# Optimization experiments

Hardware: AMD Instinct MI355X
Metric: run time of the kernel (lower is better)

## Reference

```python
import jax, jax.numpy as jnp
import numpy as np

NDIGIT = 10
DIM_IN = 256
DIM_OUT = 784
BATCH = 16384


def setup_inputs() -> dict:
    key = jax.random.key(0)
    k_theta, k_label, k_W = jax.random.split(key, 3)
    theta = jax.random.normal(k_theta, (BATCH, DIM_IN), dtype=jnp.float32)
    label = jax.random.randint(k_label, (BATCH,), 0, NDIGIT, dtype=jnp.int32)
    # xavier_uniform for each (dim_out, dim_in) matrix
    limit = float(np.sqrt(6.0 / (DIM_IN + DIM_OUT)))
    megaW = jax.random.uniform(k_W, (NDIGIT, DIM_OUT, DIM_IN), dtype=jnp.float32,
                               minval=-limit, maxval=limit)
    megab = jnp.zeros((NDIGIT, DIM_OUT), dtype=jnp.float32)
    return {"theta": theta, "label": label, "megaW": megaW, "megab": megab}


def reference(theta, label, megaW, megab):
    # Dense compute across all 10 digit experts (matches torch.bmm over repeated theta)
    # added: [b, ndigit, dim_out]
    added = jnp.einsum('ndi,bi->bnd', megaW, theta) + megab[None, :, :]
    # Select the expert output per example by label (vector_gather)
    selected = jnp.take_along_axis(added, label[:, None, None].astype(jnp.int32), axis=1)[:, 0, :]
    probs = jax.nn.sigmoid(selected)
    return probs
```

## Files before the change

kernel.cpp:

```cpp
#include <hip/hip_runtime.h>
#include <hip/hip_bf16.h>

#define NDIGIT 10
#define DIM_IN 256
#define DIM_OUT 784
#define BATCH 16384
#define BM 64
#define BN 112
#define NCB 7
#define MAX_MT (BATCH / BM + NDIGIT)
#define G_BLOCKS (MAX_MT * NCB)
#define QB 14336
#define RBSTRIDE 116
#define LDS_BYTES 29696

#define WS_IDX 1024
#define WS_DESC 600
#define WS_WBF_BYTES 69632
#define WS_TH_BYTES (WS_WBF_BYTES + 2007040 * 2)
#define WS_NEED (WS_TH_BYTES + BATCH * DIM_IN * 2)

typedef __attribute__((ext_vector_type(4))) float f32x4;
typedef __attribute__((ext_vector_type(8))) short bf16x8;

__device__ __forceinline__ short f2bf(float f) {
    union { float f; unsigned u; } c; c.f = f;
    unsigned u = c.u;
    u += 0x7fffu + ((u >> 16) & 1u);
    return (short)(u >> 16);
}

__device__ __forceinline__ void gload16(const void* gp, void* lp) {
    __builtin_amdgcn_global_load_lds(
        (const __attribute__((address_space(1))) void*)gp,
        (__attribute__((address_space(3))) void*)lp, 16, 0, 0);
}

__global__ void hist_k(const int* __restrict__ label, int* __restrict__ wsi) {
    __shared__ int h[NDIGIT];
    int j = blockIdx.x, t = threadIdx.x;
    if (t < NDIGIT) h[t] = 0;
    __syncthreads();
    int i0 = j * 512;
    atomicAdd(&h[label[i0 + t]], 1);
    atomicAdd(&h[label[i0 + 256 + t]], 1);
    __syncthreads();
    if (t < NDIGIT) wsi[64 + j * 16 + t] = h[t];
}

__global__ void scatter2_k(const int* __restrict__ label, int* __restrict__ wsi) {
    __shared__ int tot[NDIGIT], bef[NDIGIT], base[NDIGIT + 1], cur[NDIGIT], toff[NDIGIT + 1];
    int j = blockIdx.x, t = threadIdx.x;
    if (t < NDIGIT) {
        int s = 0, sb = 0;
        for (int jj = 0; jj < 32; ++jj) {
            int v = wsi[64 + jj * 16 + t];
            s += v;
            if (jj < j) sb += v;
        }
        tot[t] = s; bef[t] = sb;
    }
    __syncthreads();
    if (t == 0) {
        int off = 0, tf = 0;
        for (int g = 0; g < NDIGIT; ++g) {
            base[g] = off; toff[g] = tf;
            off += tot[g]; tf += (tot[g] + BM - 1) / BM;
        }
        base[NDIGIT] = off; toff[NDIGIT] = tf;
    }
    __syncthreads();
    if (t < NDIGIT) cur[t] = base[t] + bef[t];
    if (j == 0) {
        int ptotal = toff[NDIGIT];
        for (int p = t; p < ptotal; p += 512) {
            int g2 = 0;
            while (p >= toff[g2 + 1]) ++g2;
            int row0 = (p - toff[g2]) * BM;
            int rcv = tot[g2] - row0; if (rcv > BM) rcv = BM;
            wsi[WS_DESC + p] = (base[g2] + row0) | (rcv << 14) | (g2 << 21);
        }
        if (t < NDIGIT) { wsi[t] = base[t]; wsi[12 + t] = toff[t]; }
        if (t == 0) {
            wsi[10] = base[NDIGIT]; wsi[22] = toff[NDIGIT]; wsi[24] = toff[NDIGIT];
        }
    }
    __syncthreads();
    int i = j * 512 + t;
    int g = label[i];
    int r = atomicAdd(&cur[g], 1);
    wsi[WS_IDX + r] = i;
}

__global__ void gw_k(const float* __restrict__ theta,
                     const float* __restrict__ megaW,
                     const int* __restrict__ wsi,
                     short* __restrict__ thsort,
                     short* __restrict__ wbf) {
    int b = blockIdx.x, t = threadIdx.x;
    if (b < 2048) {
        int gid = b * 256 + t;
        int r = gid >> 5;
        int c8 = (gid & 31) << 3;
        int src = wsi[WS_IDX + r];
        const float* p = theta + (size_t)src * DIM_IN + c8;
        f32x4 v0 = *(const f32x4*)p;
        f32x4 v1 = *(const f32x4*)(p + 4);
        bf16x8 o;
        o[0] = f2bf(v0[0]); o[1] = f2bf(v0[1]); o[2] = f2bf(v0[2]); o[3] = f2bf(v0[3]);
        o[4] = f2bf(v1[0]); o[5] = f2bf(v1[1]); o[6] = f2bf(v1[2]); o[7] = f2bf(v1[3]);
        *(bf16x8*)(thsort + (size_t)r * DIM_IN + c8) = o;
    } else {
        int base = (b - 2048) * 2048 + t * 8;
        f32x4 v0 = *(const f32x4*)(megaW + base);
        f32x4 v1 = *(const f32x4*)(megaW + base + 4);
        bf16x8 o;
        o[0] = f2bf(v0[0]); o[1] = f2bf(v0[1]); o[2] = f2bf(v0[2]); o[3] = f2bf(v0[3]);
        o[4] = f2bf(v1[0]); o[5] = f2bf(v1[1]); o[6] = f2bf(v1[2]); o[7] = f2bf(v1[3]);
        *(bf16x8*)(wbf + base) = o;
    }
}

__device__ __forceinline__ void stage_q(const char* Wcb, int q, char* Bq, int tid) {
#pragma unroll
    for (int it = 0; it < 4; ++it) {
        int chunk = it * 256 + tid;
        if (chunk >= 896) chunk -= 128;
        int lbyte = chunk << 4;
        int L = lbyte ^ ((((lbyte >> 7) & 7)) << 4);
        int row = L >> 7, koff = L & 127;
        gload16(Wcb + row * 512 + q * 128 + koff, Bq + lbyte);
    }
}

#define COMPUTE_Q(Q, BUF) do {                                                 \
    _Pragma("unroll")                                                          \
    for (int ksl = 0; ksl < 2; ++ksl) {                                        \
        _Pragma("unroll")                                                      \
        for (int ns = 0; ns < NCB; ++ns) {                                     \
            int n_ = ns * 16 + r16;                                            \
            int byte_ = (n_ << 7) + (ksl << 6) + (kg << 4);                    \
            byte_ ^= (n_ & 7) << 4;                                            \
            bf16x8 bfr_ = *(const bf16x8*)((const char*)(BUF) + byte_);        \
            acc[ns] = __builtin_amdgcn_mfma_f32_16x16x32_bf16(                 \
                a[(Q) * 2 + ksl], bfr_, acc[ns], 0, 0, 0);                     \
        }                                                                      \
    }                                                                          \
} while (0)

__launch_bounds__(256, 4)
__global__ void moe_gemm11_k(const short* __restrict__ thsort,
                             const float* __restrict__ megab,
                             const int* __restrict__ wsi,
                             const short* __restrict__ wbf,
                             float* __restrict__ out) {
    __shared__ char Bs[LDS_BYTES];

    int Bid = blockIdx.x;
    const int q8 = G_BLOCKS / 8, r8 = G_BLOCKS % 8;
    int xcd = Bid & 7, slot = Bid >> 3;
    int w = (xcd < r8 ? xcd * (q8 + 1) : r8 * (q8 + 1) + (xcd - r8) * q8) + slot;
    int mt = w / NCB, cb = w % NCB;

    int total = wsi[24];
    if (mt >= total) return;

    int d = wsi[WS_DESC + mt];
    int startRow = d & 0x3FFF;
    int rc = (d >> 14) & 0x7F;
    int g  = d >> 21;

    int tid = threadIdx.x;
    int wv = tid >> 6, l = tid & 63, r16 = l & 15, kg = l >> 4;

    const char* Wcb = (const char*)(wbf + ((size_t)g * DIM_OUT + (size_t)cb * BN) * DIM_IN);

    stage_q(Wcb, 0, Bs, tid);
    stage_q(Wcb, 1, Bs + QB, tid);

    int mloc = wv * 16 + r16; if (mloc >= rc) mloc = rc - 1;
    const short* Ar = thsort + (size_t)(startRow + mloc) * DIM_IN + kg * 8;
    bf16x8 a[8];
#pragma unroll
    for (int ks = 0; ks < 8; ++ks)
        a[ks] = *(const bf16x8*)(Ar + ks * 32);

    f32x4 acc[NCB];
#pragma unroll
    for (int ns = 0; ns < NCB; ++ns) acc[ns] = (f32x4){0.f, 0.f, 0.f, 0.f};

    __syncthreads();
    COMPUTE_Q(0, Bs);
    COMPUTE_Q(1, Bs + QB);
    __syncthreads();

    stage_q(Wcb, 2, Bs, tid);
    stage_q(Wcb, 3, Bs + QB, tid);
    __syncthreads();
    COMPUTE_Q(2, Bs);
    COMPUTE_Q(3, Bs + QB);

    const float* bg = megab + (size_t)g * DIM_OUT + (size_t)cb * BN;

    __syncthreads();

    float* rowbuf = (float*)Bs + wv * (16 * RBSTRIDE);
#pragma unroll
    for (int ns = 0; ns < NCB; ++ns) {
        int nloc = ns * 16 + r16;
        float bias = bg[nloc];
#pragma unroll
        for (int j = 0; j < 4; ++j) {
            float x = acc[ns][j] + bias;
            rowbuf[(kg * 4 + j) * RBSTRIDE + nloc] = 1.0f / (1.0f + __expf(-x));
        }
    }

    __syncthreads();

    const int* idxw = wsi + WS_IDX + startRow + wv * 16;
#pragma unroll
    for (int t = 0; t < 7; ++t) {
        int c = t * 64 + l;
        int row = c / 28;
        int cir = c - row * 28;
        if (wv * 16 + row < rc) {
            f32x4 v = *(const f32x4*)(rowbuf + row * RBSTRIDE + cir * 4);
            int orow = idxw[row];
            *(f32x4*)(out + (size_t)orow * DIM_OUT + cb * BN + cir * 4) = v;
        }
    }
}

__global__ void prep_k(const float* __restrict__ megaW,
                       const int* __restrict__ label,
                       int* __restrict__ wsi,
                       short* __restrict__ wbf) {
    int b = blockIdx.x, t = threadIdx.x;
    if (b < 980) {
        int base = b * 2048 + t * 8;
        f32x4 v0 = *(const f32x4*)(megaW + base);
        f32x4 v1 = *(const f32x4*)(megaW + base + 4);
        bf16x8 o;
        o[0] = f2bf(v0[0]); o[1] = f2bf(v0[1]); o[2] = f2bf(v0[2]); o[3] = f2bf(v0[3]);
        o[4] = f2bf(v1[0]); o[5] = f2bf(v1[1]); o[6] = f2bf(v1[2]); o[7] = f2bf(v1[3]);
        *(bf16x8*)(wbf + base) = o;
    } else {
        __shared__ int h[NDIGIT];
        int j = b - 980;
        if (t < NDIGIT) h[t] = 0;
        __syncthreads();
        int i0 = j * 512;
        atomicAdd(&h[label[i0 + t]], 1);
        atomicAdd(&h[label[i0 + 256 + t]], 1);
        __syncthreads();
        if (t < NDIGIT) wsi[64 + j * 16 + t] = h[t];
    }
}

__launch_bounds__(256, 4)
__global__ void moe_gemm4_k(const float* __restrict__ theta,
                            const float* __restrict__ megab,
                            const int* __restrict__ wsi,
                            const short* __restrict__ wbf,
                            float* __restrict__ out) {
    __shared__ short Bsf[BN * 128];
    int Bid = blockIdx.x;
    const int q8 = G_BLOCKS / 8, r8 = G_BLOCKS % 8;
    int xcd = Bid & 7, slot = Bid >> 3;
    int w = (xcd < r8 ? xcd * (q8 + 1) : r8 * (q8 + 1) + (xcd - r8) * q8) + slot;
    int mt = w / NCB, cb = w % NCB;
    int total = wsi[24];
    if (mt >= total) return;
    int g = 0;
    while (mt >= wsi[12 + g + 1]) ++g;
    int lt    = mt - wsi[12 + g];
    int start = wsi[g];
    int cnt   = wsi[g + 1] - start;
    int row0  = lt * BM;
    int rc    = min(BM, cnt - row0);
    int tid = threadIdx.x;
    int wv = tid >> 6, l = tid & 63, r16 = l & 15, kg = l >> 4;
    const char* Wcb = (const char*)(wbf + ((size_t)g * DIM_OUT + (size_t)cb * BN) * DIM_IN);
#pragma unroll
    for (int it = 0; it < 7; ++it) {
        int lbyte = (it * 256 + tid) << 4;
        int L = lbyte ^ (((lbyte >> 8) & 7) << 4);
        int srcoff = ((L >> 8) << 9) + (L & 255);
        gload16(Wcb + srcoff, (char*)Bsf + lbyte);
    }
    const int* idxlist = wsi + WS_IDX + start + row0;
    int mloc = wv * 16 + r16;
    int asrc = (mloc < rc) ? idxlist[mloc] : idxlist[0];
    const float* Arow = theta + (size_t)asrc * DIM_IN;
    bf16x8 a[8];
#pragma unroll
    for (int ks = 0; ks < 8; ++ks) {
        int k0 = ks * 32 + kg * 8;
        f32x4 v0 = *(const f32x4*)(Arow + k0);
        f32x4 v1 = *(const f32x4*)(Arow + k0 + 4);
        bf16x8 af;
        af[0] = f2bf(v0[0]); af[1] = f2bf(v0[1]);
        af[2] = f2bf(v0[2]); af[3] = f2bf(v0[3]);
        af[4] = f2bf(v1[0]); af[5] = f2bf(v1[1]);
        af[6] = f2bf(v1[2]); af[7] = f2bf(v1[3]);
        a[ks] = af;
    }
    f32x4 acc[NCB];
#pragma unroll
    for (int ns = 0; ns < NCB; ++ns) acc[ns] = (f32x4){0.f, 0.f, 0.f, 0.f};
    __syncthreads();
#pragma unroll
    for (int ks = 0; ks < 4; ++ks)
#pragma unroll
        for (int ns = 0; ns < NCB; ++ns) {
            int n = ns * 16 + r16;
            int byte = (n << 8) + (ks << 6) + (kg << 4);
            byte ^= (n & 7) << 4;
            bf16x8 b = *(const bf16x8*)((const char*)Bsf + byte);
            acc[ns] = __builtin_amdgcn_mfma_f32_16x16x32_bf16(a[ks], b, acc[ns], 0, 0, 0);
        }
    __syncthreads();
#pragma unroll
    for (int it = 0; it < 7; ++it) {
        int lbyte = (it * 256 + tid) << 4;
        int L = lbyte ^ (((lbyte >> 8) & 7) << 4);
        int srcoff = ((L >> 8) << 9) + (L & 255) + 256;
        gload16(Wcb + srcoff, (char*)Bsf + lbyte);
    }
    __syncthreads();
#pragma unroll
    for (int ks = 0; ks < 4; ++ks)
#pragma unroll
        for (int ns = 0; ns < NCB; ++ns) {
            int n = ns * 16 + r16;
            int byte = (n << 8) + (ks << 6) + (kg << 4);
            byte ^= (n & 7) << 4;
            bf16x8 b = *(const bf16x8*)((const char*)Bsf + byte);
            acc[ns] = __builtin_amdgcn_mfma_f32_16x16x32_bf16(a[4 + ks], b, acc[ns], 0, 0, 0);
        }
    const float* bg = megab + (size_t)g * DIM_OUT + (size_t)cb * BN;
    int rbase = wv * 16 + kg * 4;
    int orow[4];
#pragma unroll
    for (int j = 0; j < 4; ++j)
        orow[j] = (rbase + j < rc) ? idxlist[rbase + j] : -1;
#pragma unroll
    for (int ns = 0; ns < NCB; ++ns) {
        int nloc = ns * 16 + r16;
        float bias = bg[nloc];
#pragma unroll
        for (int j = 0; j < 4; ++j) {
            if (orow[j] >= 0) {
                float x = acc[ns][j] + bias;
                out[(size_t)orow[j] * DIM_OUT + cb * BN + nloc] = 1.0f / (1.0f + __expf(-x));
            }
        }
    }
}

extern "C" void kernel_launch(void* const* d_in, const int* in_sizes, int n_in,
                              void* d_out, int out_size, void* d_ws, size_t ws_size,
                              hipStream_t stream) {
    const float* theta = (const float*)d_in[0];
    const int*   label = (const int*)d_in[1];
    const float* megaW = (const float*)d_in[2];
    const float* megab = (const float*)d_in[3];
    float* out = (float*)d_out;
    int* wsi = (int*)d_ws;
    short* wbf = (short*)((char*)d_ws + WS_WBF_BYTES);

    if (ws_size >= (size_t)WS_NEED) {
        short* thsort = (short*)((char*)d_ws + WS_TH_BYTES);
        hist_k      <<<32, 256, 0, stream>>>(label, wsi);
        scatter2_k  <<<32, 512, 0, stream>>>(label, wsi);
        gw_k        <<<3028, 256, 0, stream>>>(theta, megaW, wsi, thsort, wbf);
        moe_gemm11_k<<<G_BLOCKS, 256, 0, stream>>>(thsort, megab, wsi, wbf, out);
    } else {
        prep_k     <<<1012, 256, 0, stream>>>(megaW, label, wsi, wbf);
        scatter2_k <<<32, 512, 0, stream>>>(label, wsi);
        moe_gemm4_k<<<G_BLOCKS, 256, 0, stream>>>(theta, megab, wsi, wbf, out);
    }
}
```

Before: 43.93 us.

## Restructure grouped GEMM so each block covers all output columns for 32 rows

The main GEMM kernel now gives each 512-thread block a 32-row tile across all 784 output columns. Each wave streams pre-swizzled bf16 weight fragments straight from global memory into registers with double buffering, so the LDS weight staging and its barriers are gone. Output is packed as bf16 in LDS and written as full contiguous rows, which makes the scattered row writes coalesced. The trade-off is that each block reads the whole expert weight matrix, more tiles are padded because row tiles are smaller, outputs are rounded to bf16 before widening back to fp32, and the fallback path is rewritten with new scan and scatter kernels.

```diff
diff --git a/kernel.cpp b/kernel.cpp
--- a/kernel.cpp
+++ b/kernel.cpp
@@ -5,23 +5,20 @@
 #define DIM_IN 256
 #define DIM_OUT 784
 #define BATCH 16384
-#define BM 64
-#define BN 112
-#define NCB 7
-#define MAX_MT (BATCH / BM + NDIGIT)
-#define G_BLOCKS (MAX_MT * NCB)
-#define QB 14336
-#define RBSTRIDE 116
-#define LDS_BYTES 29696
+#define NCT 49
+#define TM32 32
+#define MAX_T32 (BATCH / TM32 + NDIGIT)
+#define RBSS 792
 
 #define WS_IDX 1024
-#define WS_DESC 600
-#define WS_WBF_BYTES 69632
+#define WS_DESC 17408
+#define WS_WBF_BYTES 81920
 #define WS_TH_BYTES (WS_WBF_BYTES + 2007040 * 2)
 #define WS_NEED (WS_TH_BYTES + BATCH * DIM_IN * 2)
 
 typedef __attribute__((ext_vector_type(4))) float f32x4;
 typedef __attribute__((ext_vector_type(8))) short bf16x8;
+typedef __attribute__((ext_vector_type(4))) unsigned short u16x4;
 
 __device__ __forceinline__ short f2bf(float f) {
     union { float f; unsigned u; } c; c.f = f;
@@ -65,7 +62,7 @@
         int off = 0, tf = 0;
         for (int g = 0; g < NDIGIT; ++g) {
             base[g] = off; toff[g] = tf;
-            off += tot[g]; tf += (tot[g] + BM - 1) / BM;
+            off += tot[g]; tf += (tot[g] + TM32 - 1) / TM32;
         }
         base[NDIGIT] = off; toff[NDIGIT] = tf;
     }
@@ -76,14 +73,12 @@
         for (int p = t; p < ptotal; p += 512) {
             int g2 = 0;
             while (p >= toff[g2 + 1]) ++g2;
-            int row0 = (p - toff[g2]) * BM;
-            int rcv = tot[g2] - row0; if (rcv > BM) rcv = BM;
+            int row0 = (p - toff[g2]) * TM32;
+            int rcv = tot[g2] - row0; if (rcv > TM32) rcv = TM32;
             wsi[WS_DESC + p] = (base[g2] + row0) | (rcv << 14) | (g2 << 21);
         }
-        if (t < NDIGIT) { wsi[t] = base[t]; wsi[12 + t] = toff[t]; }
-        if (t == 0) {
-            wsi[10] = base[NDIGIT]; wsi[22] = toff[NDIGIT]; wsi[24] = toff[NDIGIT];
-        }
+        if (t < NDIGIT) wsi[t] = base[t];
+        if (t == 0) { wsi[10] = base[NDIGIT]; wsi[24] = ptotal; }
     }
     __syncthreads();
     int i = j * 512 + t;
@@ -111,61 +106,68 @@
         o[4] = f2bf(v1[0]); o[5] = f2bf(v1[1]); o[6] = f2bf(v1[2]); o[7] = f2bf(v1[3]);
         *(bf16x8*)(thsort + (size_t)r * DIM_IN + c8) = o;
     } else {
-        int base = (b - 2048) * 2048 + t * 8;
-        f32x4 v0 = *(const f32x4*)(megaW + base);
-        f32x4 v1 = *(const f32x4*)(megaW + base + 4);
+        int idx = (b - 2048) * 256 + t;
+        int gi = idx >> 9;
+        int ks = (idx >> 6) & 7;
+        int l  = idx & 63;
+        int g  = gi / 49;
+        int ct = gi - g * 49;
+        int col = ct * 16 + (l & 15);
+        int k   = ks * 32 + ((l >> 4) << 3);
+        const float* src = megaW + ((size_t)(g * DIM_OUT + col) * DIM_IN + k);
+        f32x4 v0 = *(const f32x4*)src;
+        f32x4 v1 = *(const f32x4*)(src + 4);
         bf16x8 o;
         o[0] = f2bf(v0[0]); o[1] = f2bf(v0[1]); o[2] = f2bf(v0[2]); o[3] = f2bf(v0[3]);
         o[4] = f2bf(v1[0]); o[5] = f2bf(v1[1]); o[6] = f2bf(v1[2]); o[7] = f2bf(v1[3]);
-        *(bf16x8*)(wbf + base) = o;
-    }
-}
-
-__device__ __forceinline__ void stage_q(const char* Wcb, int q, char* Bq, int tid) {
-#pragma unroll
-    for (int it = 0; it < 4; ++it) {
-        int chunk = it * 256 + tid;
-        if (chunk >= 896) chunk -= 128;
-        int lbyte = chunk << 4;
-        int L = lbyte ^ ((((lbyte >> 7) & 7)) << 4);
-        int row = L >> 7, koff = L & 127;
-        gload16(Wcb + row * 512 + q * 128 + koff, Bq + lbyte);
-    }
-}
-
-#define COMPUTE_Q(Q, BUF) do {                                                 \
+        *(bf16x8*)(wbf + (size_t)idx * 8) = o;
+    }
+}
+
+
+#define LOADB19(B, CT) do {                                                    \
+    const short* Bt_ = Wg + (size_t)(CT) * 4096 + l * 8;                       \
     _Pragma("unroll")                                                          \
-    for (int ksl = 0; ksl < 2; ++ksl) {                                        \
-        _Pragma("unroll")                                                      \
-        for (int ns = 0; ns < NCB; ++ns) {                                     \
-            int n_ = ns * 16 + r16;                                            \
-            int byte_ = (n_ << 7) + (ksl << 6) + (kg << 4);                    \
-            byte_ ^= (n_ & 7) << 4;                                            \
-            bf16x8 bfr_ = *(const bf16x8*)((const char*)(BUF) + byte_);        \
-            acc[ns] = __builtin_amdgcn_mfma_f32_16x16x32_bf16(                 \
-                a[(Q) * 2 + ksl], bfr_, acc[ns], 0, 0, 0);                     \
-        }                                                                      \
+    for (int ks = 0; ks < 8; ++ks)                                             \
+        (B)[ks] = *(const bf16x8*)(Bt_ + ks * 512);                            \
+} while (0)
+
+#define TILE19(B, CT) do {                                                     \
+    float bias_ = bgb[(CT) * 16 + r16];                                        \
+    f32x4 A0_ = {0.f, 0.f, 0.f, 0.f}, A1_ = {0.f, 0.f, 0.f, 0.f};             \
+    _Pragma("unroll")                                                          \
+    for (int ks = 0; ks < 8; ++ks) {                                           \
+        A0_ = __builtin_amdgcn_mfma_f32_16x16x32_bf16(a0[ks], (B)[ks], A0_, 0, 0, 0); \
+        A1_ = __builtin_amdgcn_mfma_f32_16x16x32_bf16(a1[ks], (B)[ks], A1_, 0, 0, 0); \
+    }                                                                          \
+    _Pragma("unroll")                                                          \
+    for (int j = 0; j < 4; ++j) {                                              \
+        float x0_ = A0_[j] + bias_;                                            \
+        float x1_ = A1_[j] + bias_;                                            \
+        rowbuf[(kg * 4 + j) * RBSS + (CT) * 16 + r16] =                        \
+            f2bf(1.0f / (1.0f + __expf(-x0_)));                                \
+        rowbuf[(16 + kg * 4 + j) * RBSS + (CT) * 16 + r16] =                   \
+            f2bf(1.0f / (1.0f + __expf(-x1_)));                                \
     }                                                                          \
 } while (0)
 
-__launch_bounds__(256, 4)
-__global__ void moe_gemm11_k(const short* __restrict__ thsort,
+__launch_bounds__(512, 6)
+__global__ void moe_gemm19_k(const short* __restrict__ thsort,
                              const float* __restrict__ megab,
                              const int* __restrict__ wsi,
                              const short* __restrict__ wbf,
                              float* __restrict__ out) {
-    __shared__ char Bs[LDS_BYTES];
+    __shared__ short rowbuf[TM32 * RBSS];
 
     int Bid = blockIdx.x;
-    const int q8 = G_BLOCKS / 8, r8 = G_BLOCKS % 8;
+    const int q8 = MAX_T32 / 8, r8 = MAX_T32 % 8;
     int xcd = Bid & 7, slot = Bid >> 3;
-    int w = (xcd < r8 ? xcd * (q8 + 1) : r8 * (q8 + 1) + (xcd - r8) * q8) + slot;
-    int mt = w / NCB, cb = w % NCB;
+    int p = (xcd < r8 ? xcd * (q8 + 1) : r8 * (q8 + 1) + (xcd - r8) * q8) + slot;
 
     int total = wsi[24];
-    if (mt >= total) return;
-
-    int d = wsi[WS_DESC + mt];
+    if (p >= total) return;
+
+    int d = wsi[WS_DESC + p];
     int startRow = d & 0x3FFF;
     int rc = (d >> 14) & 0x7F;
     int g  = d >> 21;
@@ -173,61 +175,52 @@
     int tid = threadIdx.x;
     int wv = tid >> 6, l = tid & 63, r16 = l & 15, kg = l >> 4;
 
-    const char* Wcb = (const char*)(wbf + ((size_t)g * DIM_OUT + (size_t)cb * BN) * DIM_IN);
-
-    stage_q(Wcb, 0, Bs, tid);
-    stage_q(Wcb, 1, Bs + QB, tid);
-
-    int mloc = wv * 16 + r16; if (mloc >= rc) mloc = rc - 1;
-    const short* Ar = thsort + (size_t)(startRow + mloc) * DIM_IN + kg * 8;
-    bf16x8 a[8];
-#pragma unroll
-    for (int ks = 0; ks < 8; ++ks)
-        a[ks] = *(const bf16x8*)(Ar + ks * 32);
-
-    f32x4 acc[NCB];
-#pragma unroll
-    for (int ns = 0; ns < NCB; ++ns) acc[ns] = (f32x4){0.f, 0.f, 0.f, 0.f};
-
-    __syncthreads();
-    COMPUTE_Q(0, Bs);
-    COMPUTE_Q(1, Bs + QB);
-    __syncthreads();
-
-    stage_q(Wcb, 2, Bs, tid);
-    stage_q(Wcb, 3, Bs + QB, tid);
-    __syncthreads();
-    COMPUTE_Q(2, Bs);
-    COMPUTE_Q(3, Bs + QB);
-
-    const float* bg = megab + (size_t)g * DIM_OUT + (size_t)cb * BN;
-
-    __syncthreads();
-
-    float* rowbuf = (float*)Bs + wv * (16 * RBSTRIDE);
-#pragma unroll
-    for (int ns = 0; ns < NCB; ++ns) {
-        int nloc = ns * 16 + r16;
-        float bias = bg[nloc];
-#pragma unroll
-        for (int j = 0; j < 4; ++j) {
-            float x = acc[ns][j] + bias;
-            rowbuf[(kg * 4 + j) * RBSTRIDE + nloc] = 1.0f / (1.0f + __expf(-x));
-        }
-    }
-
-    __syncthreads();
-
-    const int* idxw = wsi + WS_IDX + startRow + wv * 16;
-#pragma unroll
-    for (int t = 0; t < 7; ++t) {
-        int c = t * 64 + l;
-        int row = c / 28;
-        int cir = c - row * 28;
-        if (wv * 16 + row < rc) {
-            f32x4 v = *(const f32x4*)(rowbuf + row * RBSTRIDE + cir * 4);
-            int orow = idxw[row];
-            *(f32x4*)(out + (size_t)orow * DIM_OUT + cb * BN + cir * 4) = v;
+    int m0 = r16;      if (m0 >= rc) m0 = rc - 1;
+    int m1 = 16 + r16; if (m1 >= rc) m1 = rc - 1;
+    const short* Ar0 = thsort + (size_t)(startRow + m0) * DIM_IN + kg * 8;
+    const short* Ar1 = thsort + (size_t)(startRow + m1) * DIM_IN + kg * 8;
+    bf16x8 a0[8], a1[8];
+#pragma unroll
+    for (int ks = 0; ks < 8; ++ks) {
+        a0[ks] = *(const bf16x8*)(Ar0 + ks * 32);
+        a1[ks] = *(const bf16x8*)(Ar1 + ks * 32);
+    }
+
+    const short* Wg  = wbf + (size_t)g * (NCT * 4096);
+    const float* bgb = megab + (size_t)g * DIM_OUT;
+
+    bf16x8 bA[8], bB[8];
+    int ct = wv;
+    LOADB19(bA, ct);
+    while (true) {
+        int c1 = ct + 8;
+        if (c1 < NCT) { LOADB19(bB, c1); TILE19(bA, ct); }
+        else          { TILE19(bA, ct); break; }
+        int c2 = c1 + 8;
+        if (c2 < NCT) { LOADB19(bA, c2); TILE19(bB, c1); }
+        else          { TILE19(bB, c1); break; }
+        ct = c2;
+    }
+
+    __syncthreads();
+
+    const int* idxl = wsi + WS_IDX + startRow;
+#pragma unroll
+    for (int s = 0; s < 13; ++s) {
+        int c = s * 512 + tid;
+        if (c < TM32 * 196) {
+            int row = c / 196;
+            int cir = c - row * 196;
+            if (row < rc) {
+                u16x4 v = *(const u16x4*)(rowbuf + row * RBSS + cir * 4);
+                union { unsigned u; float f; } c0, c1, c2, c3;
+                c0.u = (unsigned)v[0] << 16;
+                c1.u = (unsigned)v[1] << 16;
+                c2.u = (unsigned)v[2] << 16;
+                c3.u = (unsigned)v[3] << 16;
+                f32x4 o = { c0.f, c1.f, c2.f, c3.f };
+                *(f32x4*)(out + (size_t)idxl[row] * DIM_OUT + cir * 4) = o;
+            }
         }
     }
 }
@@ -258,30 +251,54 @@
     }
 }
 
+__global__ void fscan_k(int* __restrict__ wsi) {
+    int off = 0, toff = 0;
+    for (int g = 0; g < NDIGIT; ++g) {
+        int tot = 0;
+        for (int jj = 0; jj < 32; ++jj) tot += wsi[64 + jj * 16 + g];
+        wsi[g] = off;
+        wsi[40 + g] = toff;
+        off += tot;
+        toff += (tot + 63) / 64;
+    }
+    wsi[10] = off; wsi[50] = toff; wsi[24] = toff;
+}
+
+__global__ void fscatter_k(const int* __restrict__ label, int* __restrict__ wsi) {
+    __shared__ int lc[NDIGIT], lb[NDIGIT];
+    int t = threadIdx.x;
+    if (t < NDIGIT) lc[t] = 0;
+    __syncthreads();
+    int i = blockIdx.x * 256 + t;
+    int g = label[i];
+    int r = atomicAdd(&lc[g], 1);
+    __syncthreads();
+    if (t < NDIGIT) lb[t] = (lc[t] > 0) ? atomicAdd(&wsi[52 + t], lc[t]) : 0;
+    __syncthreads();
+    wsi[WS_IDX + wsi[g] + lb[g] + r] = i;
+}
+
 __launch_bounds__(256, 4)
-__global__ void moe_gemm4_k(const float* __restrict__ theta,
+__global__ void moe_gemmF_k(const float* __restrict__ theta,
                             const float* __restrict__ megab,
                             const int* __restrict__ wsi,
                             const short* __restrict__ wbf,
                             float* __restrict__ out) {
-    __shared__ short Bsf[BN * 128];
+    __shared__ short Bsf[112 * 128];
     int Bid = blockIdx.x;
-    const int q8 = G_BLOCKS / 8, r8 = G_BLOCKS % 8;
-    int xcd = Bid & 7, slot = Bid >> 3;
-    int w = (xcd < r8 ? xcd * (q8 + 1) : r8 * (q8 + 1) + (xcd - r8) * q8) + slot;
-    int mt = w / NCB, cb = w % NCB;
+    int mt = Bid / 7, cb = Bid % 7;
     int total = wsi[24];
     if (mt >= total) return;
     int g = 0;
-    while (mt >= wsi[12 + g + 1]) ++g;
-    int lt    = mt - wsi[12 + g];
+    while (mt >= wsi[40 + g + 1]) ++g;
+    int lt    = mt - wsi[40 + g];
     int start = wsi[g];
     int cnt   = wsi[g + 1] - start;
-    int row0  = lt * BM;
-    int rc    = min(BM, cnt - row0);
+    int row0  = lt * 64;
+    int rc    = min(64, cnt - row0);
     int tid = threadIdx.x;
     int wv = tid >> 6, l = tid & 63, r16 = l & 15, kg = l >> 4;
-    const char* Wcb = (const char*)(wbf + ((size_t)g * DIM_OUT + (size_t)cb * BN) * DIM_IN);
+    const char* Wcb = (const char*)(wbf + ((size_t)g * DIM_OUT + (size_t)cb * 112) * DIM_IN);
 #pragma unroll
     for (int it = 0; it < 7; ++it) {
         int lbyte = (it * 256 + tid) << 4;
@@ -306,14 +323,14 @@
         af[6] = f2bf(v1[2]); af[7] = f2bf(v1[3]);
         a[ks] = af;
     }
-    f32x4 acc[NCB];
-#pragma unroll
-    for (int ns = 0; ns < NCB; ++ns) acc[ns] = (f32x4){0.f, 0.f, 0.f, 0.f};
+    f32x4 acc[7];
+#pragma unroll
+    for (int ns = 0; ns < 7; ++ns) acc[ns] = (f32x4){0.f, 0.f, 0.f, 0.f};
     __syncthreads();
 #pragma unroll
     for (int ks = 0; ks < 4; ++ks)
 #pragma unroll
-        for (int ns = 0; ns < NCB; ++ns) {
+        for (int ns = 0; ns < 7; ++ns) {
             int n = ns * 16 + r16;
             int byte = (n << 8) + (ks << 6) + (kg << 4);
             byte ^= (n & 7) << 4;
@@ -332,28 +349,28 @@
 #pragma unroll
     for (int ks = 0; ks < 4; ++ks)
 #pragma unroll
-        for (int ns = 0; ns < NCB; ++ns) {
+        for (int ns = 0; ns < 7; ++ns) {
             int n = ns * 16 + r16;
             int byte = (n << 8) + (ks << 6) + (kg << 4);
             byte ^= (n & 7) << 4;
             bf16x8 b = *(const bf16x8*)((const char*)Bsf + byte);
             acc[ns] = __builtin_amdgcn_mfma_f32_16x16x32_bf16(a[4 + ks], b, acc[ns], 0, 0, 0);
         }
-    const float* bg = megab + (size_t)g * DIM_OUT + (size_t)cb * BN;
+    const float* bg = megab + (size_t)g * DIM_OUT + (size_t)cb * 112;
     int rbase = wv * 16 + kg * 4;
     int orow[4];
 #pragma unroll
     for (int j = 0; j < 4; ++j)
         orow[j] = (rbase + j < rc) ? idxlist[rbase + j] : -1;
 #pragma unroll
-    for (int ns = 0; ns < NCB; ++ns) {
+    for (int ns = 0; ns < 7; ++ns) {
         int nloc = ns * 16 + r16;
         float bias = bg[nloc];
 #pragma unroll
         for (int j = 0; j < 4; ++j) {
             if (orow[j] >= 0) {
                 float x = acc[ns][j] + bias;
-                out[(size_t)orow[j] * DIM_OUT + cb * BN + nloc] = 1.0f / (1.0f + __expf(-x));
+                out[(size_t)orow[j] * DIM_OUT + cb * 112 + nloc] = 1.0f / (1.0f + __expf(-x));
             }
         }
     }
@@ -375,10 +392,12 @@
         hist_k      <<<32, 256, 0, stream>>>(label, wsi);
         scatter2_k  <<<32, 512, 0, stream>>>(label, wsi);
         gw_k        <<<3028, 256, 0, stream>>>(theta, megaW, wsi, thsort, wbf);
-        moe_gemm11_k<<<G_BLOCKS, 256, 0, stream>>>(thsort, megab, wsi, wbf, out);
+        moe_gemm19_k<<<MAX_T32, 512, 0, stream>>>(thsort, megab, wsi, wbf, out);
     } else {
+        hipMemsetAsync((char*)d_ws + 52 * 4, 0, 10 * 4, stream);
         prep_k     <<<1012, 256, 0, stream>>>(megaW, label, wsi, wbf);
-        scatter2_k <<<32, 512, 0, stream>>>(label, wsi);
-        moe_gemm4_k<<<G_BLOCKS, 256, 0, stream>>>(theta, megab, wsi, wbf, out);
-    }
-}
+        fscan_k    <<<1, 1, 0, stream>>>(wsi);
+        fscatter_k <<<64, 256, 0, stream>>>(label, wsi);
+        moe_gemmF_k<<<274 * 7, 256, 0, stream>>>(theta, megab, wsi, wbf, out);
+    }
+}
```

Measured after the change: 132.4 us. 3.01x slower.
